# Optimization experiments

Hardware: AMD Instinct MI355X
Metric: run time of the kernel (lower is better)

The kernel has to match this reference:

```python
import jax, jax.numpy as jnp
import numpy as np

EPS = 1e-5


def _bn(x, g, b, m, v):
    # eval-mode BatchNorm over the last (channel) axis
    return g * (x - m) * jax.lax.rsqrt(v + EPS) + b


def setup_inputs() -> dict:
    key = jax.random.key(0)
    ks = jax.random.split(key, 16)
    B, N, K, C, Cout, G = 2, 16384, 32, 64, 64, 10
    inp = {
        "points": jax.random.normal(ks[0], (B, N, 3), jnp.float32),
        "features": jax.random.normal(ks[1], (B, N, C), jnp.float32),
        "grouped_idx": jax.random.randint(ks[2], (B, N, K), 0, N, jnp.int32),
        # pos_proj: Conv2d(geo_ch, in_ch, 1) + BN + ReLU
        "W_pos": jax.random.normal(ks[3], (C, G), jnp.float32) / np.sqrt(G),
        "b_pos": jnp.zeros((C,), jnp.float32),
        "bn1_g": jnp.ones((C,), jnp.float32),
        "bn1_b": jnp.zeros((C,), jnp.float32),
        "bn1_m": jax.random.normal(ks[4], (C,), jnp.float32) * 0.1,
        "bn1_v": jax.random.uniform(ks[5], (C,), jnp.float32, 0.5, 1.5),
        # gcm_layer: Conv2d(in_ch, in_ch, 1) + BN + ReLU
        "W_gcm": jax.random.normal(ks[6], (C, C), jnp.float32) / np.sqrt(C),
        "b_gcm": jnp.zeros((C,), jnp.float32),
        "bn2_g": jnp.ones((C,), jnp.float32),
        "bn2_b": jnp.zeros((C,), jnp.float32),
        "bn2_m": jax.random.normal(ks[7], (C,), jnp.float32) * 0.1,
        "bn2_v": jax.random.uniform(ks[8], (C,), jnp.float32, 0.5, 1.5),
        # att_conv_catfea: Linear(nsample, 1)
        "W_att": jax.random.normal(ks[9], (K,), jnp.float32) / np.sqrt(K),
        "b_att": jnp.zeros((), jnp.float32),
        # out_layer: Linear(in_ch, out_ch) + LayerNorm + ReLU
        "W_out": jax.random.normal(ks[10], (Cout, C), jnp.float32) / np.sqrt(C),
        "b_out": jnp.zeros((Cout,), jnp.float32),
        "ln_g": jnp.ones((Cout,), jnp.float32),
        "ln_b": jnp.zeros((Cout,), jnp.float32),
    }
    return inp


def reference(points, features, grouped_idx, W_pos, b_pos, bn1_g, bn1_b, bn1_m, bn1_v,
              W_gcm, b_gcm, bn2_g, bn2_b, bn2_m, bn2_v, W_att, b_att,
              W_out, b_out, ln_g, ln_b):
    gather = jax.vmap(lambda arr, idx: arr[idx])  # [N,C],[N,K] -> [N,K,C]
    grouped_points = gather(points, grouped_idx)          # [B,N,K,3]
    grouped_f = gather(features, grouped_idx)             # [B,N,K,C]

    # legacy geometric encoding: [xi, xj, xi - xj, ||xi - xj||] -> geo_ch = 10
    xi = points[:, :, None, :]
    diff = xi - grouped_points
    dist = jnp.linalg.norm(diff, axis=-1, keepdims=True)
    geo = jnp.concatenate(
        [jnp.broadcast_to(xi, grouped_points.shape), grouped_points, diff, dist], axis=-1)

    # pos_proj: 1x1 conv == channel linear, + BN + ReLU
    expanded = jax.nn.relu(_bn(jnp.einsum('bnkg,cg->bnkc', geo, W_pos) + b_pos,
                               bn1_g, bn1_b, bn1_m, bn1_v))

    h = grouped_f + expanded
    # gcm_layer
    h = jax.nn.relu(_bn(jnp.einsum('bnkc,dc->bnkd', h, W_gcm) + b_gcm,
                        bn2_g, bn2_b, bn2_m, bn2_v))

    # attention over neighbor dim K -> score per channel, softmax over channels (dim=2 of [B,N,C,1])
    score = jnp.einsum('bnkc,k->bnc', h, W_att) + b_att   # [B,N,C]
    score = jax.nn.softmax(score, axis=-1)
    h = h * score[:, :, None, :]                          # [B,N,K,C]

    pooled = jnp.max(h, axis=2)                           # maxpooling downsample -> [B,N,C]
    res = pooled + features

    # out_layer: Linear + LayerNorm + ReLU
    y = jnp.einsum('bnc,oc->bno', res, W_out) + b_out
    mu = jnp.mean(y, axis=-1, keepdims=True)
    var = jnp.var(y, axis=-1, keepdims=True)
    y = ln_g * (y - mu) * jax.lax.rsqrt(var + EPS) + ln_b
    return jax.nn.relu(y)
```

## Files before the change

kernel.cpp:

```cpp
#include <hip/hip_runtime.h>
#include <hip/hip_bf16.h>

#define EPSF 1e-5f

typedef __attribute__((ext_vector_type(8))) short bf16x8;
typedef __attribute__((ext_vector_type(4))) float f32x4;
typedef __attribute__((ext_vector_type(2))) unsigned int u32x2;
typedef __attribute__((ext_vector_type(4))) unsigned int u32x4;
typedef __attribute__((ext_vector_type(4))) int i32x4;

constexpr int B_ = 2, N_ = 16384;
constexpr int HSTR = 72;
constexpr int RSTR = 72;
constexpr int PPW  = 8;
constexpr int NW   = 8;
constexpr int PPB  = 64;
constexpr int NWG  = (B_ * N_) / PPB;
constexpr int HALF = NWG / 2;
constexpr size_t PP_BYTES = (size_t)B_ * N_ * 16;

__device__ __forceinline__ short f2bf(float f) {
    __hip_bfloat16 h = __float2bfloat16(f);
    short s; __builtin_memcpy(&s, &h, 2); return s;
}
__device__ __forceinline__ unsigned int pkbf(float a, float b) {
    float2 f2; f2.x = a; f2.y = b;
    __hip_bfloat162 h = __float22bfloat162_rn(f2);
    unsigned int u; __builtin_memcpy(&u, &h, 4); return u;
}

__global__ __launch_bounds__(256) void prep_points(
    const float* __restrict__ pts, float* __restrict__ pp)
{
    const int i = blockIdx.x * 256 + threadIdx.x;
    if (i < B_ * N_) {
        f32x4 o = { pts[3 * i], pts[3 * i + 1], pts[3 * i + 2], 0.f };
        ((f32x4*)pp)[i] = o;
    }
}

template<bool PAD>
__global__ __launch_bounds__(512, 2) void bridgenet11(
    const float* __restrict__ points,
    const float* __restrict__ pp,
    const float* __restrict__ features,
    const int*   __restrict__ gidx,
    const float* __restrict__ Wpos,
    const float* __restrict__ bposv,
    const float* __restrict__ bn1g, const float* __restrict__ bn1b,
    const float* __restrict__ bn1m, const float* __restrict__ bn1v,
    const float* __restrict__ Wgcm,
    const float* __restrict__ bgcm,
    const float* __restrict__ bn2g, const float* __restrict__ bn2b,
    const float* __restrict__ bn2m, const float* __restrict__ bn2v,
    const float* __restrict__ Watt,
    const float* __restrict__ batt,
    const float* __restrict__ Wout,
    const float* __restrict__ bout,
    const float* __restrict__ lng, const float* __restrict__ lnb,
    float* __restrict__ out)
{
    __shared__ __align__(16) short hbuf[NW][32 * HSTR];
    __shared__ __align__(16) short resstage[PPB * RSTR];
    __shared__ __align__(16) short wb2[8 * 64 * 8];
    __shared__ __align__(16) short wb3[8 * 64 * 8];

    const int t    = threadIdx.x;
    const int w    = t >> 6;
    const int l    = t & 63;
    const int l15  = l & 15;
    const int quad = l >> 4;
    const int c4   = l15 * 4;

    const int wg  = blockIdx.x;
    const int blk = ((wg & 7) >> 2) * HALF + ((wg >> 3) << 2) + (wg & 3);

    {
        #pragma unroll
        for (int u = 0; u < 2; ++u) {
            const int s  = w * 2 + u;
            const int nt = (s >> 1) & 3, ks = s & 1;
            const float* src = (s < 8 ? Wgcm : Wout) + (c4 + nt) * 64 + ks * 32 + quad * 8;
            const f32x4 w0 = *(const f32x4*)src;
            const f32x4 w1 = *(const f32x4*)(src + 4);
            bf16x8 f;
            #pragma unroll
            for (int j = 0; j < 4; ++j) {
                f[j]     = f2bf(w0[j]);
                f[j + 4] = f2bf(w1[j]);
            }
            short* dst = (s < 8 ? wb2 : wb3);
            *(bf16x8*)&dst[((s & 7) * 64 + l) * 8] = f;
        }
    }

    bf16x8 bposf[4];
    #pragma unroll
    for (int nt = 0; nt < 4; ++nt) {
        const int c = c4 + nt;
        #pragma unroll
        for (int j = 0; j < 8; ++j) {
            const int g = quad * 8 + j;
            bposf[nt][j] = f2bf(g < 10 ? Wpos[c * 10 + g] : 0.f);
        }
    }
    f32x4 ps1, pb1, ps2, pb2;
    {
        const f32x4 g1 = *(const f32x4*)(bn1g + c4);
        const f32x4 b1 = *(const f32x4*)(bn1b + c4);
        const f32x4 m1 = *(const f32x4*)(bn1m + c4);
        const f32x4 v1 = *(const f32x4*)(bn1v + c4);
        const f32x4 bp = *(const f32x4*)(bposv + c4);
        const f32x4 g2 = *(const f32x4*)(bn2g + c4);
        const f32x4 b2 = *(const f32x4*)(bn2b + c4);
        const f32x4 m2 = *(const f32x4*)(bn2m + c4);
        const f32x4 v2 = *(const f32x4*)(bn2v + c4);
        const f32x4 bg = *(const f32x4*)(bgcm + c4);
        #pragma unroll
        for (int j = 0; j < 4; ++j) {
            ps1[j] = g1[j] * rsqrtf(v1[j] + EPSF);
            pb1[j] = ps1[j] * (bp[j] - m1[j]) + b1[j];
            ps2[j] = g2[j] * rsqrtf(v2[j] + EPSF);
            pb2[j] = ps2[j] * (bg[j] - m2[j]) + b2[j];
        }
    }
    float wat[2][4];
    #pragma unroll
    for (int mt = 0; mt < 2; ++mt)
        #pragma unroll
        for (int r = 0; r < 4; ++r)
            wat[mt][r] = Watt[mt * 16 + quad * 4 + r];
    const float battv = batt[0];

    const f32x4 zero4 = {0.f, 0.f, 0.f, 0.f};
    short* hb = hbuf[w];
    const int base = blk * PPB + w * PPW;
    const int bb   = ((blk * PPB) >> 14) * N_;

    auto LOADI = [&](int pt, i32x4 (&gi)[2]) {
        gi[0] = *(const i32x4*)(gidx + (size_t)pt * 32 + quad * 4);
        gi[1] = *(const i32x4*)(gidx + (size_t)pt * 32 + 16 + quad * 4);
    };
    auto LOADD = [&](int pt, const i32x4 (&gi)[2],
                     f32x4 (&f4)[2][4], bf16x8 (&ageo)[2], f32x4& resid) {
        #pragma unroll
        for (int mt = 0; mt < 2; ++mt)
            #pragma unroll
            for (int r = 0; r < 4; ++r)
                f4[mt][r] = *(const f32x4*)(features + (size_t)(bb + gi[mt][r]) * 64 + c4);
        resid = *(const f32x4*)(features + (size_t)pt * 64 + c4);
        int gv[2];
        gv[0] = gidx[(size_t)pt * 32 + l15];
        gv[1] = gidx[(size_t)pt * 32 + 16 + l15];
        float xi0, xi1, xi2, px[2], py[2], pz[2];
        if (PAD) {
            const f32x4 x4 = *(const f32x4*)(pp + (size_t)pt * 4);
            xi0 = x4[0]; xi1 = x4[1]; xi2 = x4[2];
            #pragma unroll
            for (int mt = 0; mt < 2; ++mt) {
                const f32x4 p4 = *(const f32x4*)(pp + (size_t)(bb + gv[mt]) * 4);
                px[mt] = p4[0]; py[mt] = p4[1]; pz[mt] = p4[2];
            }
        } else {
            xi0 = points[(size_t)pt * 3];
            xi1 = points[(size_t)pt * 3 + 1];
            xi2 = points[(size_t)pt * 3 + 2];
            #pragma unroll
            for (int mt = 0; mt < 2; ++mt) {
                const float* ppt = points + (size_t)(bb + gv[mt]) * 3;
                px[mt] = ppt[0]; py[mt] = ppt[1]; pz[mt] = ppt[2];
            }
        }
        #pragma unroll
        for (int mt = 0; mt < 2; ++mt) {
            const float dx = xi0 - px[mt], dy = xi1 - py[mt], dz = xi2 - pz[mt];
            const float dist = sqrtf(dx * dx + dy * dy + dz * dz);
            u32x4 u = {0u, 0u, 0u, 0u};
            if (quad == 0) {
                u[0] = pkbf(xi0, xi1); u[1] = pkbf(xi2, px[mt]);
                u[2] = pkbf(py[mt], pz[mt]); u[3] = pkbf(dx, dy);
            } else if (quad == 1) {
                u[0] = pkbf(dz, dist);
            }
            __builtin_memcpy(&ageo[mt], &u, 16);
        }
    };

    i32x4 giC[2], giN[2];
    LOADI(base, giC);
    LOADI(base + 1, giN);
    f32x4  f4c[2][4];
    bf16x8 ageoc[2];
    f32x4  residc;
    LOADD(base, giC, f4c, ageoc, residc);

    __syncthreads();

    #pragma unroll 2
    for (int i = 0; i < PPW; ++i) {
        f32x4  f4n[2][4];
        bf16x8 ageon[2];
        f32x4  residn;
        i32x4  giN2[2];
        if (i + 1 < PPW) LOADD(base + i + 1, giN, f4n, ageon, residn);
        if (i + 2 < PPW) LOADI(base + i + 2, giN2);

        __builtin_amdgcn_s_setprio(1);
        f32x4 acc1[2][4];
        #pragma unroll
        for (int mt = 0; mt < 2; ++mt)
            #pragma unroll
            for (int nt = 0; nt < 4; ++nt)
                acc1[mt][nt] = __builtin_amdgcn_mfma_f32_16x16x32_bf16(
                    ageoc[mt], bposf[nt], zero4, 0, 0, 0);
        __builtin_amdgcn_s_setprio(0);

        #pragma unroll
        for (int mt = 0; mt < 2; ++mt)
            #pragma unroll
            for (int r = 0; r < 4; ++r) {
                const int k = mt * 16 + quad * 4 + r;
                float v[4];
                #pragma unroll
                for (int j = 0; j < 4; ++j)
                    v[j] = f4c[mt][r][j] + fmaxf(ps1[j] * acc1[mt][j][r] + pb1[j], 0.f);
                u32x2 hv = { pkbf(v[0], v[1]), pkbf(v[2], v[3]) };
                *(u32x2*)&hb[k * HSTR + c4] = hv;
            }

        bf16x8 a2[2][2];
        #pragma unroll
        for (int mt = 0; mt < 2; ++mt)
            #pragma unroll
            for (int ks = 0; ks < 2; ++ks)
                a2[mt][ks] = *(const bf16x8*)&hb[(mt * 16 + l15) * HSTR + ks * 32 + quad * 8];
        __builtin_amdgcn_s_setprio(1);
        f32x4 acc2[2][4];
        #pragma unroll
        for (int nt = 0; nt < 4; ++nt) {
            const bf16x8 b0 = *(const bf16x8*)&wb2[((nt * 2 + 0) * 64 + l) * 8];
            const bf16x8 b1 = *(const bf16x8*)&wb2[((nt * 2 + 1) * 64 + l) * 8];
            #pragma unroll
            for (int mt = 0; mt < 2; ++mt) {
                f32x4 a = __builtin_amdgcn_mfma_f32_16x16x32_bf16(a2[mt][0], b0, zero4, 0, 0, 0);
                acc2[mt][nt] = __builtin_amdgcn_mfma_f32_16x16x32_bf16(a2[mt][1], b1, a, 0, 0, 0);
            }
        }
        __builtin_amdgcn_s_setprio(0);

        float res[4];
        {
            float sp[4], mk[4];
            #pragma unroll
            for (int nt = 0; nt < 4; ++nt) {
                sp[nt] = 0.f; mk[nt] = 0.f;
                #pragma unroll
                for (int mt = 0; mt < 2; ++mt)
                    #pragma unroll
                    for (int r = 0; r < 4; ++r) {
                        const float h2 = fmaxf(ps2[nt] * acc2[mt][nt][r] + pb2[nt], 0.f);
                        sp[nt] += h2 * wat[mt][r];
                        mk[nt] = fmaxf(mk[nt], h2);
                    }
                sp[nt] += __shfl_xor(sp[nt], 16);
                sp[nt] += __shfl_xor(sp[nt], 32);
                mk[nt] = fmaxf(mk[nt], __shfl_xor(mk[nt], 16));
                mk[nt] = fmaxf(mk[nt], __shfl_xor(mk[nt], 32));
            }
            float e[4], s = 0.f;
            #pragma unroll
            for (int nt = 0; nt < 4; ++nt) { e[nt] = __expf(sp[nt] + battv); s += e[nt]; }
            #pragma unroll
            for (int o = 1; o < 16; o <<= 1) s += __shfl_xor(s, o);
            const float inv = 1.f / s;
            #pragma unroll
            for (int nt = 0; nt < 4; ++nt)
                res[nt] = e[nt] * inv * mk[nt] + residc[nt];
        }
        if (quad == 0) {
            u32x2 rv = { pkbf(res[0], res[1]), pkbf(res[2], res[3]) };
            *(u32x2*)&resstage[(w * PPW + i) * RSTR + c4] = rv;
        }

        if (i + 1 < PPW) {
            #pragma unroll
            for (int mt = 0; mt < 2; ++mt) {
                #pragma unroll
                for (int r = 0; r < 4; ++r) f4c[mt][r] = f4n[mt][r];
                ageoc[mt] = ageon[mt];
            }
            residc = residn;
            if (i + 2 < PPW) { giN[0] = giN2[0]; giN[1] = giN2[1]; }
        }
    }

    __syncthreads();

    {
        const int g = w >> 1;
        const f32x4 lngv  = *(const f32x4*)(lng + c4);
        const f32x4 lnbv  = *(const f32x4*)(lnb + c4);
        const f32x4 boutv = *(const f32x4*)(bout + c4);
        bf16x8 a3[2];
        #pragma unroll
        for (int ks = 0; ks < 2; ++ks)
            a3[ks] = *(const bf16x8*)&resstage[(g * 16 + l15) * RSTR + ks * 32 + quad * 8];
        f32x4 acc3[4];
        #pragma unroll
        for (int nt = 0; nt < 4; ++nt) {
            const bf16x8 b0 = *(const bf16x8*)&wb3[((nt * 2 + 0) * 64 + l) * 8];
            const bf16x8 b1 = *(const bf16x8*)&wb3[((nt * 2 + 1) * 64 + l) * 8];
            f32x4 a = __builtin_amdgcn_mfma_f32_16x16x32_bf16(a3[0], b0, zero4, 0, 0, 0);
            acc3[nt] = __builtin_amdgcn_mfma_f32_16x16x32_bf16(a3[1], b1, a, 0, 0, 0);
        }
        #pragma unroll
        for (int u = 0; u < 2; ++u) {
            const int r = (w & 1) * 2 + u;
            float y[4], s = 0.f;
            #pragma unroll
            for (int nt = 0; nt < 4; ++nt) { y[nt] = acc3[nt][r] + boutv[nt]; s += y[nt]; }
            #pragma unroll
            for (int o = 1; o < 16; o <<= 1) s += __shfl_xor(s, o);
            const float mu = s * (1.f / 64.f);
            float dv[4], v2 = 0.f;
            #pragma unroll
            for (int nt = 0; nt < 4; ++nt) { dv[nt] = y[nt] - mu; v2 += dv[nt] * dv[nt]; }
            #pragma unroll
            for (int o = 1; o < 16; o <<= 1) v2 += __shfl_xor(v2, o);
            const float rs = rsqrtf(v2 * (1.f / 64.f) + EPSF);
            const int pto = blk * PPB + g * 16 + quad * 4 + r;
            f32x4 ov;
            #pragma unroll
            for (int nt = 0; nt < 4; ++nt)
                ov[nt] = fmaxf(lngv[nt] * dv[nt] * rs + lnbv[nt], 0.f);
            *(f32x4*)(out + (size_t)pto * 64 + c4) = ov;
        }
    }
}

extern "C" void kernel_launch(void* const* d_in, const int* in_sizes, int n_in,
                              void* d_out, int out_size, void* d_ws, size_t ws_size,
                              hipStream_t stream) {
    const float* points   = (const float*)d_in[0];
    const float* features = (const float*)d_in[1];
    const int*   gidxp    = (const int*)d_in[2];
    const bool   pad      = (ws_size >= PP_BYTES);
    float* pp = (float*)d_ws;
    if (pad) {
        hipLaunchKernelGGL(prep_points, dim3((B_ * N_ + 255) / 256), dim3(256), 0, stream,
                           points, pp);
        hipLaunchKernelGGL((bridgenet11<true>), dim3(NWG), dim3(512), 0, stream,
            points, pp, features, gidxp,
            (const float*)d_in[3],  (const float*)d_in[4],
            (const float*)d_in[5],  (const float*)d_in[6],  (const float*)d_in[7],  (const float*)d_in[8],
            (const float*)d_in[9],  (const float*)d_in[10],
            (const float*)d_in[11], (const float*)d_in[12], (const float*)d_in[13], (const float*)d_in[14],
            (const float*)d_in[15], (const float*)d_in[16],
            (const float*)d_in[17], (const float*)d_in[18],
            (const float*)d_in[19], (const float*)d_in[20],
            (float*)d_out);
    } else {
        hipLaunchKernelGGL((bridgenet11<false>), dim3(NWG), dim3(512), 0, stream,
            points, pp, features, gidxp,
            (const float*)d_in[3],  (const float*)d_in[4],
            (const float*)d_in[5],  (const float*)d_in[6],  (const float*)d_in[7],  (const float*)d_in[8],
            (const float*)d_in[9],  (const float*)d_in[10],
            (const float*)d_in[11], (const float*)d_in[12], (const float*)d_in[13], (const float*)d_in[14],
            (const float*)d_in[15], (const float*)d_in[16],
            (const float*)d_in[17], (const float*)d_in[18],
            (const float*)d_in[19], (const float*)d_in[20],
            (float*)d_out);
    }
}
```

Baseline: 163.3 us.

## Double points per workgroup and share one LDS weight buffer across GEMM stages

Each workgroup now handles 128 points (16 per wave) instead of 64, halving the grid and amortizing per-block setup such as weight conversion, bias/BN loads and the output-stage sync. The two separate LDS weight buffers are merged into one: Wgcm is staged first, then after the main loop Wout is loaded into the same buffer behind an extra barrier. The output GEMM is reorganized so each wave handles a 16-point tile and all four rows. Fewer blocks on a larger resstage may reduce load balance or occupancy, and the extra Wout load and barrier add latency to the epilogue.

```diff
diff --git a/kernel.cpp b/kernel.cpp
--- a/kernel.cpp
+++ b/kernel.cpp
@@ -12,9 +12,9 @@
 constexpr int B_ = 2, N_ = 16384;
 constexpr int HSTR = 72;
 constexpr int RSTR = 72;
-constexpr int PPW  = 8;
+constexpr int PPW  = 16;
 constexpr int NW   = 8;
-constexpr int PPB  = 64;
+constexpr int PPB  = 128;
 constexpr int NWG  = (B_ * N_) / PPB;
 constexpr int HALF = NWG / 2;
 constexpr size_t PP_BYTES = (size_t)B_ * N_ * 16;
@@ -40,7 +40,7 @@
 }
 
 template<bool PAD>
-__global__ __launch_bounds__(512, 2) void bridgenet11(
+__global__ __launch_bounds__(512, 2) void bridgenet12(
     const float* __restrict__ points,
     const float* __restrict__ pp,
     const float* __restrict__ features,
@@ -62,8 +62,7 @@
 {
     __shared__ __align__(16) short hbuf[NW][32 * HSTR];
     __shared__ __align__(16) short resstage[PPB * RSTR];
-    __shared__ __align__(16) short wb2[8 * 64 * 8];
-    __shared__ __align__(16) short wb3[8 * 64 * 8];
+    __shared__ __align__(16) short wb[8 * 64 * 8];
 
     const int t    = threadIdx.x;
     const int w    = t >> 6;
@@ -76,22 +75,17 @@
     const int blk = ((wg & 7) >> 2) * HALF + ((wg >> 3) << 2) + (wg & 3);
 
     {
-        #pragma unroll
-        for (int u = 0; u < 2; ++u) {
-            const int s  = w * 2 + u;
-            const int nt = (s >> 1) & 3, ks = s & 1;
-            const float* src = (s < 8 ? Wgcm : Wout) + (c4 + nt) * 64 + ks * 32 + quad * 8;
-            const f32x4 w0 = *(const f32x4*)src;
-            const f32x4 w1 = *(const f32x4*)(src + 4);
-            bf16x8 f;
-            #pragma unroll
-            for (int j = 0; j < 4; ++j) {
-                f[j]     = f2bf(w0[j]);
-                f[j + 4] = f2bf(w1[j]);
-            }
-            short* dst = (s < 8 ? wb2 : wb3);
-            *(bf16x8*)&dst[((s & 7) * 64 + l) * 8] = f;
-        }
+        const int nt = w >> 1, ks = w & 1;
+        const float* src = Wgcm + (c4 + nt) * 64 + ks * 32 + quad * 8;
+        const f32x4 w0 = *(const f32x4*)src;
+        const f32x4 w1 = *(const f32x4*)(src + 4);
+        bf16x8 f;
+        #pragma unroll
+        for (int j = 0; j < 4; ++j) {
+            f[j]     = f2bf(w0[j]);
+            f[j + 4] = f2bf(w1[j]);
+        }
+        *(bf16x8*)&wb[(w * 64 + l) * 8] = f;
     }
 
     bf16x8 bposf[4];
@@ -238,8 +232,8 @@
         f32x4 acc2[2][4];
         #pragma unroll
         for (int nt = 0; nt < 4; ++nt) {
-            const bf16x8 b0 = *(const bf16x8*)&wb2[((nt * 2 + 0) * 64 + l) * 8];
-            const bf16x8 b1 = *(const bf16x8*)&wb2[((nt * 2 + 1) * 64 + l) * 8];
+            const bf16x8 b0 = *(const bf16x8*)&wb[((nt * 2 + 0) * 64 + l) * 8];
+            const bf16x8 b1 = *(const bf16x8*)&wb[((nt * 2 + 1) * 64 + l) * 8];
             #pragma unroll
             for (int mt = 0; mt < 2; ++mt) {
                 f32x4 a = __builtin_amdgcn_mfma_f32_16x16x32_bf16(a2[mt][0], b0, zero4, 0, 0, 0);
@@ -297,28 +291,42 @@
     __syncthreads();
 
     {
-        const int g = w >> 1;
+        const int nt = w >> 1, ks = w & 1;
+        const float* src = Wout + (c4 + nt) * 64 + ks * 32 + quad * 8;
+        const f32x4 w0 = *(const f32x4*)src;
+        const f32x4 w1 = *(const f32x4*)(src + 4);
+        bf16x8 f;
+        #pragma unroll
+        for (int j = 0; j < 4; ++j) {
+            f[j]     = f2bf(w0[j]);
+            f[j + 4] = f2bf(w1[j]);
+        }
+        *(bf16x8*)&wb[(w * 64 + l) * 8] = f;
+    }
+
+    __syncthreads();
+
+    {
         const f32x4 lngv  = *(const f32x4*)(lng + c4);
         const f32x4 lnbv  = *(const f32x4*)(lnb + c4);
         const f32x4 boutv = *(const f32x4*)(bout + c4);
         bf16x8 a3[2];
         #pragma unroll
         for (int ks = 0; ks < 2; ++ks)
-            a3[ks] = *(const bf16x8*)&resstage[(g * 16 + l15) * RSTR + ks * 32 + quad * 8];
+            a3[ks] = *(const bf16x8*)&resstage[(w * 16 + l15) * RSTR + ks * 32 + quad * 8];
         f32x4 acc3[4];
         #pragma unroll
         for (int nt = 0; nt < 4; ++nt) {
-            const bf16x8 b0 = *(const bf16x8*)&wb3[((nt * 2 + 0) * 64 + l) * 8];
-            const bf16x8 b1 = *(const bf16x8*)&wb3[((nt * 2 + 1) * 64 + l) * 8];
+            const bf16x8 b0 = *(const bf16x8*)&wb[((nt * 2 + 0) * 64 + l) * 8];
+            const bf16x8 b1 = *(const bf16x8*)&wb[((nt * 2 + 1) * 64 + l) * 8];
             f32x4 a = __builtin_amdgcn_mfma_f32_16x16x32_bf16(a3[0], b0, zero4, 0, 0, 0);
             acc3[nt] = __builtin_amdgcn_mfma_f32_16x16x32_bf16(a3[1], b1, a, 0, 0, 0);
         }
         #pragma unroll
-        for (int u = 0; u < 2; ++u) {
-            const int r = (w & 1) * 2 + u;
+        for (int u = 0; u < 4; ++u) {
             float y[4], s = 0.f;
             #pragma unroll
-            for (int nt = 0; nt < 4; ++nt) { y[nt] = acc3[nt][r] + boutv[nt]; s += y[nt]; }
+            for (int nt = 0; nt < 4; ++nt) { y[nt] = acc3[nt][u] + boutv[nt]; s += y[nt]; }
             #pragma unroll
             for (int o = 1; o < 16; o <<= 1) s += __shfl_xor(s, o);
             const float mu = s * (1.f / 64.f);
@@ -328,7 +336,7 @@
             #pragma unroll
             for (int o = 1; o < 16; o <<= 1) v2 += __shfl_xor(v2, o);
             const float rs = rsqrtf(v2 * (1.f / 64.f) + EPSF);
-            const int pto = blk * PPB + g * 16 + quad * 4 + r;
+            const int pto = blk * PPB + w * 16 + quad * 4 + u;
             f32x4 ov;
             #pragma unroll
             for (int nt = 0; nt < 4; ++nt)
@@ -349,7 +357,7 @@
     if (pad) {
         hipLaunchKernelGGL(prep_points, dim3((B_ * N_ + 255) / 256), dim3(256), 0, stream,
                            points, pp);
-        hipLaunchKernelGGL((bridgenet11<true>), dim3(NWG), dim3(512), 0, stream,
+        hipLaunchKernelGGL((bridgenet12<true>), dim3(NWG), dim3(512), 0, stream,
             points, pp, features, gidxp,
             (const float*)d_in[3],  (const float*)d_in[4],
             (const float*)d_in[5],  (const float*)d_in[6],  (const float*)d_in[7],  (const float*)d_in[8],
@@ -360,7 +368,7 @@
             (const float*)d_in[19], (const float*)d_in[20],
             (float*)d_out);
     } else {
-        hipLaunchKernelGGL((bridgenet11<false>), dim3(NWG), dim3(512), 0, stream,
+        hipLaunchKernelGGL((bridgenet12<false>), dim3(NWG), dim3(512), 0, stream,
             points, pp, features, gidxp,
             (const float*)d_in[3],  (const float*)d_in[4],
             (const float*)d_in[5],  (const float*)d_in[6],  (const float*)d_in[7],  (const float*)d_in[8],
```

Result: faster. 155.1 us (-5.0%).
